# Performance work log

Hardware: AMD Instinct MI355X
Metric: run time of the kernel (lower is better)

Reference implementation:

```python
import jax, jax.numpy as jnp
import numpy as np

OUT = 128
TYPES = [("author", 100000, 128), ("paper", 250000, 256), ("venue", 25000, 64),
         ("institution", 50000, 128), ("field", 75000, 64), ("term", 150000, 128)]


def setup_inputs() -> dict:
    key = jax.random.key(0)
    inp = {}
    for i, (name, n, f_in) in enumerate(TYPES):
        kx, kw, kb = jax.random.split(jax.random.fold_in(key, i), 3)
        inp[f"x_{name}"] = jax.random.normal(kx, (n, f_in), dtype=jnp.float32)
        # kaiming_uniform default init of torch Linear: bound = 1/sqrt(fan_in)
        bound = 1.0 / np.sqrt(f_in)
        inp[f"W_{name}"] = jax.random.uniform(kw, (OUT, f_in), dtype=jnp.float32, minval=-bound, maxval=bound)
        inp[f"b_{name}"] = jax.random.uniform(kb, (OUT,), dtype=jnp.float32, minval=-bound, maxval=bound)
    return inp


def reference(x_author, x_paper, x_venue, x_institution, x_field, x_term,
              W_author, b_author, W_paper, b_paper, W_venue, b_venue,
              W_institution, b_institution, W_field, b_field, W_term, b_term):
    # Per-type independent Linear: y_k = x_k @ W_k^T + b_k (grouped GEMM)
    def lin(x, W, b):
        return jnp.einsum('nf,of->no', x, W) + b
    return (lin(x_author, W_author, b_author),
            lin(x_paper, W_paper, b_paper),
            lin(x_venue, W_venue, b_venue),
            lin(x_institution, W_institution, b_institution),
            lin(x_field, W_field, b_field),
            lin(x_term, W_term, b_term))
```

## Files before the change

kernel.cpp:

```cpp
#include <hip/hip_runtime.h>

typedef __bf16 bf16x4 __attribute__((ext_vector_type(4)));
typedef __bf16 bf16x8 __attribute__((ext_vector_type(8)));
typedef float  f32x4  __attribute__((ext_vector_type(4)));

struct KArgs {
    const float* x[6];
    const float* W[6];
    const float* b[6];
    float*       out[6];
    int nrows[6];
    int blk0[7];
};

__device__ __forceinline__ void lds_barrier() {
    asm volatile("s_waitcnt lgkmcnt(0)\n\ts_barrier" ::: "memory");
}

template<int FIN>
__device__ __forceinline__ void run_type(
    const float* __restrict__ x, const float* __restrict__ W,
    const float* __restrict__ bias, float* __restrict__ out,
    int nrows, int c0, int c1, __bf16* __restrict__ lds)
{
    constexpr int ROWS = 4096 / FIN;
    constexpr int NC   = FIN / 32;
    constexpr int MT   = ROWS / 16;
    constexpr int S    = FIN * 2;
    constexpr int QPR  = FIN / 4;

    const int tid     = threadIdx.x;
    const int lane    = tid & 63;
    const int wave    = tid >> 6;
    const int l15     = lane & 15;
    const int lq      = lane >> 4;
    const int colbase = wave * 32;

    bf16x8 Wf[NC][2];
    f32x4  bv[2];
    #pragma unroll
    for (int t = 0; t < 2; ++t) {
        const int o = colbase + t * 16 + l15;
        #pragma unroll
        for (int c = 0; c < NC; ++c) {
            const f32x4 w0 = *(const f32x4*)(W + (size_t)o * FIN + c * 32 + lq * 8);
            const f32x4 w1 = *(const f32x4*)(W + (size_t)o * FIN + c * 32 + lq * 8 + 4);
            bf16x8 fr;
            fr[0] = (__bf16)w0[0]; fr[1] = (__bf16)w0[1];
            fr[2] = (__bf16)w0[2]; fr[3] = (__bf16)w0[3];
            fr[4] = (__bf16)w1[0]; fr[5] = (__bf16)w1[1];
            fr[6] = (__bf16)w1[2]; fr[7] = (__bf16)w1[3];
            Wf[c][t] = fr;
        }
        bv[t] = *(const f32x4*)(bias + colbase + t * 16 + lq * 4);
    }

    f32x4 fbuf[4];

    auto issue = [&](int chunk) {
        #pragma unroll
        for (int i = 0; i < 4; ++i) {
            const int u  = tid + i * 256;
            const int r  = u / QPR;
            const int kq = u % QPR;
            int gr = chunk * ROWS + r;
            if (gr >= nrows) gr = nrows - 1;
            fbuf[i] = __builtin_nontemporal_load(
                (const f32x4*)(x + (size_t)gr * FIN + kq * 4));
        }
    };
    auto commit = [&](int b) {
        __bf16* dst = lds + b * 4096;
        #pragma unroll
        for (int i = 0; i < 4; ++i) {
            const int u  = tid + i * 256;
            const int r  = u / QPR;
            const int kq = u % QPR;
            bf16x4 q;
            q[0] = (__bf16)fbuf[i][0]; q[1] = (__bf16)fbuf[i][1];
            q[2] = (__bf16)fbuf[i][2]; q[3] = (__bf16)fbuf[i][3];
            const int byte = (r * S + kq * 8) ^ ((r & 7) << 4);
            *(bf16x4*)((char*)dst + byte) = q;
        }
    };

    issue(c0);
    commit(0);
    lds_barrier();

    int cur = 0;
    for (int n = c0; n < c1; ++n) {
        const bool more = (n + 1 < c1);
        if (more) issue(n + 1);

        const __bf16* src = lds + cur * 4096;
        #pragma unroll
        for (int mt = 0; mt < MT; ++mt) {
            const int row = mt * 16 + l15;
            f32x4 acc0 = {0.f, 0.f, 0.f, 0.f};
            f32x4 acc1 = {0.f, 0.f, 0.f, 0.f};
            #pragma unroll
            for (int c = 0; c < NC; ++c) {
                const int byte = (row * S + c * 64 + lq * 16) ^ ((row & 7) << 4);
                const bf16x8 xf = *(const bf16x8*)((const char*)src + byte);
                acc0 = __builtin_amdgcn_mfma_f32_16x16x32_bf16(Wf[c][0], xf, acc0, 0, 0, 0);
                acc1 = __builtin_amdgcn_mfma_f32_16x16x32_bf16(Wf[c][1], xf, acc1, 0, 0, 0);
            }
            const int xrow = n * ROWS + mt * 16 + l15;
            if (xrow < nrows) {
                float* op = out + (size_t)xrow * 128 + colbase;
                __builtin_nontemporal_store(acc0 + bv[0], (f32x4*)(op + lq * 4));
                __builtin_nontemporal_store(acc1 + bv[1], (f32x4*)(op + 16 + lq * 4));
            }
        }

        if (more) commit(cur ^ 1);
        lds_barrier();
        cur ^= 1;
    }
}

__global__ __launch_bounds__(256, 2) void hetero_fused_kern(KArgs A)
{
    __shared__ __bf16 lds[2 * 4096];

    int ty = 0;
    const int bid = blockIdx.x;
    while (ty < 5 && bid >= A.blk0[ty + 1]) ++ty;
    const int lb = bid - A.blk0[ty];
    const int nb = A.blk0[ty + 1] - A.blk0[ty];

    const int nrows  = A.nrows[ty];
    const int ROWS   = (ty == 1) ? 16 : ((ty == 2 || ty == 4) ? 64 : 32);
    const int chunks = (nrows + ROWS - 1) / ROWS;
    const int c0 = (int)(((long)chunks * lb) / nb);
    const int c1 = (int)(((long)chunks * (lb + 1)) / nb);
    if (c0 >= c1) return;

    switch (ty) {
        case 0: run_type<128>(A.x[0], A.W[0], A.b[0], A.out[0], nrows, c0, c1, lds); break;
        case 1: run_type<256>(A.x[1], A.W[1], A.b[1], A.out[1], nrows, c0, c1, lds); break;
        case 2: run_type< 64>(A.x[2], A.W[2], A.b[2], A.out[2], nrows, c0, c1, lds); break;
        case 3: run_type<128>(A.x[3], A.W[3], A.b[3], A.out[3], nrows, c0, c1, lds); break;
        case 4: run_type< 64>(A.x[4], A.W[4], A.b[4], A.out[4], nrows, c0, c1, lds); break;
        case 5: run_type<128>(A.x[5], A.W[5], A.b[5], A.out[5], nrows, c0, c1, lds); break;
    }
}

extern "C" void kernel_launch(void* const* d_in, const int* in_sizes, int n_in,
                              void* d_out, int out_size, void* d_ws, size_t ws_size,
                              hipStream_t stream)
{
    float* out = (float*)d_out;
    KArgs A;
    const int  nrows[6] = {100000, 250000, 25000, 50000, 75000, 150000};
    const long ooff[6]  = {0L, 12800000L, 44800000L, 48000000L, 54400000L, 64000000L};
    const int  blk0[7]  = {0, 273, 1297, 1348, 1485, 1639, 2048};
    for (int t = 0; t < 6; ++t) {
        A.x[t]     = (const float*)d_in[3 * t + 0];
        A.W[t]     = (const float*)d_in[3 * t + 1];
        A.b[t]     = (const float*)d_in[3 * t + 2];
        A.out[t]   = out + ooff[t];
        A.nrows[t] = nrows[t];
    }
    for (int i = 0; i < 7; ++i) A.blk0[i] = blk0[i];

    hetero_fused_kern<<<2048, 256, 0, stream>>>(A);
}
```

Baseline: 171.9 us.

## Stream activations into LDS via direct global-to-LDS loads with triple buffering

Replaces the register-staged load, convert-to-bf16 and LDS store path with global_load_lds, which writes fp32 rows directly into a swizzled LDS layout. Uses a three-buffer ring synchronised with vmcnt-based barriers, so up to two chunks are in flight while one is computed. The bf16 conversion moves to the point of reading from LDS. Partial trailing chunks go through a separate guarded path on the last block, and launch bounds rise to 3 blocks per CU. In exchange, LDS per block doubles to 48KB because it holds fp32 tiles, and the vmcnt counts are hand-tuned, which is fragile if the compiler emits other memory ops in between.

```diff
diff --git a/kernel.cpp b/kernel.cpp
--- a/kernel.cpp
+++ b/kernel.cpp
@@ -1,6 +1,5 @@
 #include <hip/hip_runtime.h>
 
-typedef __bf16 bf16x4 __attribute__((ext_vector_type(4)));
 typedef __bf16 bf16x8 __attribute__((ext_vector_type(8)));
 typedef float  f32x4  __attribute__((ext_vector_type(4)));
 
@@ -13,21 +12,65 @@
     int blk0[7];
 };
 
-__device__ __forceinline__ void lds_barrier() {
-    asm volatile("s_waitcnt lgkmcnt(0)\n\ts_barrier" ::: "memory");
+template<int N> __device__ __forceinline__ void wait_bar() {
+    asm volatile("s_waitcnt vmcnt(%0)\n\ts_barrier" :: "n"(N) : "memory");
+}
+__device__ __forceinline__ void order_fence() { asm volatile("" ::: "memory"); }
+
+__device__ __forceinline__ void gload_lds16(const float* g, void* l) {
+    __builtin_amdgcn_global_load_lds(
+        (const __attribute__((address_space(1))) void*)g,
+        (__attribute__((address_space(3))) void*)l, 16, 0, 0);
+}
+
+template<int FIN, bool GUARD>
+__device__ __forceinline__ void compute_chunk(
+    const char* __restrict__ base, const bf16x8 (&Wf)[FIN/32][2],
+    const f32x4 (&bv)[2], float* __restrict__ out, int nrows, int chunk,
+    int l15, int lq, int colbase)
+{
+    constexpr int ROWS = 4096 / FIN;
+    constexpr int NC   = FIN / 32;
+    constexpr int MT   = ROWS / 16;
+    constexpr int R    = FIN / 4;
+    #pragma unroll
+    for (int mt = 0; mt < MT; ++mt) {
+        const int row = mt * 16 + l15;
+        const int swz = row & 7;
+        f32x4 acc0 = {0.f, 0.f, 0.f, 0.f};
+        f32x4 acc1 = {0.f, 0.f, 0.f, 0.f};
+        #pragma unroll
+        for (int c = 0; c < NC; ++c) {
+            const int g0 = row * R + c * 8 + lq * 2;
+            const f32x4 lo = *(const f32x4*)(base + (size_t)((g0 ^ swz) << 4));
+            const f32x4 hi = *(const f32x4*)(base + (size_t)(((g0 + 1) ^ swz) << 4));
+            bf16x8 xf;
+            xf[0]=(__bf16)lo[0]; xf[1]=(__bf16)lo[1]; xf[2]=(__bf16)lo[2]; xf[3]=(__bf16)lo[3];
+            xf[4]=(__bf16)hi[0]; xf[5]=(__bf16)hi[1]; xf[6]=(__bf16)hi[2]; xf[7]=(__bf16)hi[3];
+            acc0 = __builtin_amdgcn_mfma_f32_16x16x32_bf16(Wf[c][0], xf, acc0, 0, 0, 0);
+            acc1 = __builtin_amdgcn_mfma_f32_16x16x32_bf16(Wf[c][1], xf, acc1, 0, 0, 0);
+        }
+        const int xrow = chunk * ROWS + mt * 16 + l15;
+        if (!GUARD || xrow < nrows) {
+            float* op = out + (size_t)xrow * 128 + colbase;
+            __builtin_nontemporal_store(acc0 + bv[0], (f32x4*)(op + lq * 4));
+            __builtin_nontemporal_store(acc1 + bv[1], (f32x4*)(op + 16 + lq * 4));
+        }
+    }
 }
 
 template<int FIN>
 __device__ __forceinline__ void run_type(
     const float* __restrict__ x, const float* __restrict__ W,
     const float* __restrict__ bias, float* __restrict__ out,
-    int nrows, int c0, int c1, __bf16* __restrict__ lds)
+    int nrows, int c0, int c1, bool tail, float* __restrict__ lds)
 {
     constexpr int ROWS = 4096 / FIN;
     constexpr int NC   = FIN / 32;
     constexpr int MT   = ROWS / 16;
-    constexpr int S    = FIN * 2;
-    constexpr int QPR  = FIN / 4;
+    constexpr int R    = FIN / 4;
+    constexpr int S    = 2 * MT;
+    constexpr int LOGR = (FIN == 256) ? 6 : ((FIN == 128) ? 5 : 4);
 
     const int tid     = threadIdx.x;
     const int lane    = tid & 63;
@@ -46,83 +89,75 @@
             const f32x4 w0 = *(const f32x4*)(W + (size_t)o * FIN + c * 32 + lq * 8);
             const f32x4 w1 = *(const f32x4*)(W + (size_t)o * FIN + c * 32 + lq * 8 + 4);
             bf16x8 fr;
-            fr[0] = (__bf16)w0[0]; fr[1] = (__bf16)w0[1];
-            fr[2] = (__bf16)w0[2]; fr[3] = (__bf16)w0[3];
-            fr[4] = (__bf16)w1[0]; fr[5] = (__bf16)w1[1];
-            fr[6] = (__bf16)w1[2]; fr[7] = (__bf16)w1[3];
+            fr[0]=(__bf16)w0[0]; fr[1]=(__bf16)w0[1]; fr[2]=(__bf16)w0[2]; fr[3]=(__bf16)w0[3];
+            fr[4]=(__bf16)w1[0]; fr[5]=(__bf16)w1[1]; fr[6]=(__bf16)w1[2]; fr[7]=(__bf16)w1[3];
             Wf[c][t] = fr;
         }
         bv[t] = *(const f32x4*)(bias + colbase + t * 16 + lq * 4);
     }
 
-    f32x4 fbuf[4];
-
-    auto issue = [&](int chunk) {
+    auto issue = [&](int chunk, int b) {
+        const float* src = x + (size_t)chunk * ROWS * FIN;
         #pragma unroll
         for (int i = 0; i < 4; ++i) {
-            const int u  = tid + i * 256;
-            const int r  = u / QPR;
-            const int kq = u % QPR;
-            int gr = chunk * ROWS + r;
-            if (gr >= nrows) gr = nrows - 1;
-            fbuf[i] = __builtin_nontemporal_load(
-                (const f32x4*)(x + (size_t)gr * FIN + kq * 4));
+            const int G   = wave * 256 + i * 64 + lane;
+            const int row = G >> LOGR;
+            const int kq  = (G & (R - 1)) ^ (row & 7);
+            gload_lds16(src + (size_t)row * FIN + kq * 4,
+                        (char*)lds + (size_t)b * 16384 + wave * 4096 + i * 1024);
         }
     };
-    auto commit = [&](int b) {
-        __bf16* dst = lds + b * 4096;
+
+    const int L = c1 - c0;
+    if (L > 0) {
+        const int last = c1 - 1;
+        order_fence();
+        issue(c0, 0);
+        int ch1 = c0 + 1; if (ch1 > last) ch1 = last;
+        issue(ch1, 1);
+        wait_bar<4>();
+        int ch2 = c0 + 2; if (ch2 > last) ch2 = last;
+        issue(ch2, 2);
+        order_fence();
+        compute_chunk<FIN, false>((const char*)lds, Wf, bv, out, nrows, c0,
+                                  l15, lq, colbase);
+        if (L > 1) {
+            wait_bar<4 + S>();
+            for (int k = 1; k < L; ++k) {
+                int ch = c0 + k + 2; if (ch > last) ch = last;
+                issue(ch, (k + 2) % 3);
+                order_fence();
+                compute_chunk<FIN, false>((const char*)lds + (size_t)(k % 3) * 16384,
+                                          Wf, bv, out, nrows, c0 + k,
+                                          l15, lq, colbase);
+                if (k + 1 < L) wait_bar<4 + 2 * S>();
+            }
+        }
+    }
+
+    if (tail) {
+        __syncthreads();
+        const int pc = c1;
         #pragma unroll
         for (int i = 0; i < 4; ++i) {
-            const int u  = tid + i * 256;
-            const int r  = u / QPR;
-            const int kq = u % QPR;
-            bf16x4 q;
-            q[0] = (__bf16)fbuf[i][0]; q[1] = (__bf16)fbuf[i][1];
-            q[2] = (__bf16)fbuf[i][2]; q[3] = (__bf16)fbuf[i][3];
-            const int byte = (r * S + kq * 8) ^ ((r & 7) << 4);
-            *(bf16x4*)((char*)dst + byte) = q;
-        }
-    };
-
-    issue(c0);
-    commit(0);
-    lds_barrier();
-
-    int cur = 0;
-    for (int n = c0; n < c1; ++n) {
-        const bool more = (n + 1 < c1);
-        if (more) issue(n + 1);
-
-        const __bf16* src = lds + cur * 4096;
-        #pragma unroll
-        for (int mt = 0; mt < MT; ++mt) {
-            const int row = mt * 16 + l15;
-            f32x4 acc0 = {0.f, 0.f, 0.f, 0.f};
-            f32x4 acc1 = {0.f, 0.f, 0.f, 0.f};
-            #pragma unroll
-            for (int c = 0; c < NC; ++c) {
-                const int byte = (row * S + c * 64 + lq * 16) ^ ((row & 7) << 4);
-                const bf16x8 xf = *(const bf16x8*)((const char*)src + byte);
-                acc0 = __builtin_amdgcn_mfma_f32_16x16x32_bf16(Wf[c][0], xf, acc0, 0, 0, 0);
-                acc1 = __builtin_amdgcn_mfma_f32_16x16x32_bf16(Wf[c][1], xf, acc1, 0, 0, 0);
+            const int G   = wave * 256 + i * 64 + lane;
+            const int row = G >> LOGR;
+            const int kq  = (G & (R - 1)) ^ (row & 7);
+            const int grow = pc * ROWS + row;
+            if (grow < nrows) {
+                const f32x4 v = *(const f32x4*)(x + (size_t)grow * FIN + kq * 4);
+                *(f32x4*)((char*)lds + (size_t)G * 16) = v;
             }
-            const int xrow = n * ROWS + mt * 16 + l15;
-            if (xrow < nrows) {
-                float* op = out + (size_t)xrow * 128 + colbase;
-                __builtin_nontemporal_store(acc0 + bv[0], (f32x4*)(op + lq * 4));
-                __builtin_nontemporal_store(acc1 + bv[1], (f32x4*)(op + 16 + lq * 4));
-            }
-        }
-
-        if (more) commit(cur ^ 1);
-        lds_barrier();
-        cur ^= 1;
-    }
-}
-
-__global__ __launch_bounds__(256, 2) void hetero_fused_kern(KArgs A)
-{
-    __shared__ __bf16 lds[2 * 4096];
+        }
+        __syncthreads();
+        compute_chunk<FIN, true>((const char*)lds, Wf, bv, out, nrows, pc,
+                                 l15, lq, colbase);
+    }
+}
+
+__global__ __launch_bounds__(256, 3) void hetero_fused_kern(KArgs A)
+{
+    __shared__ float lds[3 * 4096];
 
     int ty = 0;
     const int bid = blockIdx.x;
@@ -130,20 +165,21 @@
     const int lb = bid - A.blk0[ty];
     const int nb = A.blk0[ty + 1] - A.blk0[ty];
 
-    const int nrows  = A.nrows[ty];
-    const int ROWS   = (ty == 1) ? 16 : ((ty == 2 || ty == 4) ? 64 : 32);
-    const int chunks = (nrows + ROWS - 1) / ROWS;
-    const int c0 = (int)(((long)chunks * lb) / nb);
-    const int c1 = (int)(((long)chunks * (lb + 1)) / nb);
-    if (c0 >= c1) return;
+    const int nrows = A.nrows[ty];
+    const int ROWS  = (ty == 1) ? 16 : ((ty == 2 || ty == 4) ? 64 : 32);
+    const int F     = nrows / ROWS;
+    const bool part = (nrows % ROWS) != 0;
+    const int c0 = (int)(((long)F * lb) / nb);
+    const int c1 = (int)(((long)F * (lb + 1)) / nb);
+    const bool tail = part && (lb == nb - 1);
 
     switch (ty) {
-        case 0: run_type<128>(A.x[0], A.W[0], A.b[0], A.out[0], nrows, c0, c1, lds); break;
-        case 1: run_type<256>(A.x[1], A.W[1], A.b[1], A.out[1], nrows, c0, c1, lds); break;
-        case 2: run_type< 64>(A.x[2], A.W[2], A.b[2], A.out[2], nrows, c0, c1, lds); break;
-        case 3: run_type<128>(A.x[3], A.W[3], A.b[3], A.out[3], nrows, c0, c1, lds); break;
-        case 4: run_type< 64>(A.x[4], A.W[4], A.b[4], A.out[4], nrows, c0, c1, lds); break;
-        case 5: run_type<128>(A.x[5], A.W[5], A.b[5], A.out[5], nrows, c0, c1, lds); break;
+        case 0: run_type<128>(A.x[0], A.W[0], A.b[0], A.out[0], nrows, c0, c1, tail, lds); break;
+        case 1: run_type<256>(A.x[1], A.W[1], A.b[1], A.out[1], nrows, c0, c1, tail, lds); break;
+        case 2: run_type< 64>(A.x[2], A.W[2], A.b[2], A.out[2], nrows, c0, c1, tail, lds); break;
+        case 3: run_type<128>(A.x[3], A.W[3], A.b[3], A.out[3], nrows, c0, c1, tail, lds); break;
+        case 4: run_type< 64>(A.x[4], A.W[4], A.b[4], A.out[4], nrows, c0, c1, tail, lds); break;
+        case 5: run_type<128>(A.x[5], A.W[5], A.b[5], A.out[5], nrows, c0, c1, tail, lds); break;
     }
 }
 
```

After: 175.8 us, median of 3. 1.02x slower.
